# Kernel optimization log

Hardware: AMD Instinct MI355X
Metric: run time of the kernel (lower is better)

Reference implementation:

```python
import jax, jax.numpy as jnp
import numpy as np

N = 50000; E = 400000; T = 8; CIN = 16; C = 32; L = 2
F = C * T; END = 128; G = 64; EPS = 1e-5


def conv1d(x, W, b, pad):
    # x: (N, Cin, T), W: (Cout, Cin, K) -> (N, Cout, T)  ('same' padding)
    y = jax.lax.conv_general_dilated(x, W, (1,), [(pad, pad)],
                                     dimension_numbers=('NCH', 'OIH', 'NCH'))
    return y + b[None, :, None]


def gated_conv(x, W3, b3):
    # Temporal_Gated_Conv: relu(conv1(x) * sigmoid(conv2(x)) + conv3(x))
    P = conv1d(x, W3[0], b3[0], 1)
    Q = jax.nn.sigmoid(conv1d(x, W3[1], b3[1], 1))
    R = conv1d(x, W3[2], b3[2], 1)
    return jax.nn.relu(P * Q + R)


def bn(x, g, b, axes):
    # BatchNorm in training mode (batch statistics), channel axis = 1
    m = jnp.mean(x, axis=axes, keepdims=True)
    v = jnp.var(x, axis=axes, keepdims=True)
    sh = [1] * x.ndim; sh[1] = -1
    return (x - m) * jax.lax.rsqrt(v + EPS) * g.reshape(sh) + b.reshape(sh)


def gcn(x, W, b, src, dst):
    # GCNConv with self-loops (already appended to src/dst) and symmetric norm
    h = x @ W  # transform first: (N, F)
    deg = jax.ops.segment_sum(jnp.ones(src.shape[0], x.dtype), dst, num_segments=N)
    dinv = jnp.where(deg > 0, jax.lax.rsqrt(jnp.maximum(deg, 1.0)), 0.0)
    norm = dinv[src] * dinv[dst]  # (E+N,)
    out = jax.ops.segment_sum(h[src] * norm[:, None], dst, num_segments=N)
    return out + b


def stgcn_forward(X, edge_index, graphs, W_in, b_in, res_W, res_b, g1_W, g1_b,
                  bn0_g, bn0_b, gcn_W, gcn_b, bn1_g, bn1_b, g2_W, g2_b,
                  bn2_g, bn2_b, out_W1, out_b1, out_W2, out_b2, out_W3, out_b3):
    loop = jnp.arange(N)
    src = jnp.concatenate([edge_index[0], loop])
    dst = jnp.concatenate([edge_index[1], loop])
    x = conv1d(X, W_in, b_in, 0)  # input 1x1 conv -> (N, C, T)
    for i in range(L):
        residual = conv1d(x, res_W[i], res_b[i], 0)
        h = gated_conv(x, g1_W[i], g1_b[i])
        h = bn(h, bn0_g[i], bn0_b[i], (0, 2))
        h = h.reshape(N, F)                      # view(N, n_seq * C) row-major
        h = gcn(h, gcn_W[i], gcn_b[i], src, dst)
        h = bn(h, bn1_g[i], bn1_b[i], (0,))
        h = h.reshape(N, C, T)
        h = gated_conv(h, g2_W[i], g2_b[i])
        h = bn(h, bn2_g[i], bn2_b[i], (0, 2))
        h = h + residual
        if i != L - 1:                            # last layer skips activation
            h = jax.nn.relu(h)
        x = h
    # graph mode: take last timestep, then mean/max/sum pool per graph
    xl = x[:, :, -1]  # (N, C)
    cnt = jax.ops.segment_sum(jnp.ones((N,), xl.dtype), graphs, num_segments=G)
    s = jax.ops.segment_sum(xl, graphs, num_segments=G)
    mean = s / jnp.maximum(cnt, 1.0)[:, None]
    mx = jax.ops.segment_max(xl, graphs, num_segments=G)
    mx = jnp.where(cnt[:, None] > 0, mx, 0.0)
    xg = jnp.concatenate([mean, mx, s], axis=1)  # (G, 3C)
    h = jax.nn.relu(xg @ out_W1 + out_b1)
    h = jax.nn.relu(h @ out_W2 + out_b2)
    return h @ out_W3 + out_b3  # (G, 1)


def setup_inputs() -> dict:
    key = jax.random.key(0)
    ks = jax.random.split(key, 12)
    s = 0.1
    return {
        'X': jax.random.normal(ks[0], (N, CIN, T), jnp.float32),
        'edge_index': jax.random.randint(ks[1], (2, E), 0, N),
        'graphs': jnp.sort(jax.random.randint(ks[2], (N,), 0, G)),
        'W_in': jax.random.normal(ks[3], (C, CIN, 1)) * s,
        'b_in': jnp.zeros((C,)),
        'res_W': jax.random.normal(ks[4], (L, C, C, 1)) * s,
        'res_b': jnp.zeros((L, C)),
        'g1_W': jax.random.normal(ks[5], (L, 3, C, C, 3)) * s,
        'g1_b': jnp.zeros((L, 3, C)),
        'bn0_g': jnp.ones((L, C)), 'bn0_b': jnp.zeros((L, C)),
        'gcn_W': jax.random.normal(ks[6], (L, F, F)) * np.float32(1.0 / np.sqrt(F)),
        'gcn_b': jnp.zeros((L, F)),
        'bn1_g': jnp.ones((L, F)), 'bn1_b': jnp.zeros((L, F)),
        'g2_W': jax.random.normal(ks[7], (L, 3, C, C, 3)) * s,
        'g2_b': jnp.zeros((L, 3, C)),
        'bn2_g': jnp.ones((L, C)), 'bn2_b': jnp.zeros((L, C)),
        'out_W1': jax.random.normal(ks[8], (3 * C, END)) * s,
        'out_b1': jnp.zeros((END,)),
        'out_W2': jax.random.normal(ks[9], (END, END // 2)) * s,
        'out_b2': jnp.zeros((END // 2,)),
        'out_W3': jax.random.normal(ks[10], (END // 2, 1)) * s,
        'out_b3': jnp.zeros((1,)),
    }


def reference(X, edge_index, graphs, W_in, b_in, res_W, res_b, g1_W, g1_b,
              bn0_g, bn0_b, gcn_W, gcn_b, bn1_g, bn1_b, g2_W, g2_b,
              bn2_g, bn2_b, out_W1, out_b1, out_W2, out_b2, out_W3, out_b3):
    return stgcn_forward(X, edge_index, graphs, W_in, b_in, res_W, res_b,
                         g1_W, g1_b, bn0_g, bn0_b, gcn_W, gcn_b, bn1_g, bn1_b,
                         g2_W, g2_b, bn2_g, bn2_b, out_W1, out_b1, out_W2,
                         out_b2, out_W3, out_b3)
```

## Files before the change

### kernel.cpp

```cpp
#include <hip/hip_runtime.h>
#include <hip/hip_bf16.h>

#define NN 50000
#define EE 400000
#define EPSF 1e-5f
#define NB 196
#define NGATED 1280

typedef unsigned short u16;
typedef __attribute__((ext_vector_type(8))) short bf16x8;
typedef __attribute__((ext_vector_type(4))) float f32x4;
typedef __attribute__((ext_vector_type(2))) float f32x2;

__device__ __forceinline__ float b2f(u16 u) { return __uint_as_float(((unsigned)u) << 16); }
__device__ __forceinline__ u16 f2b(float f) {
  unsigned x = __float_as_uint(f);
  unsigned r = x + 0x7FFFu + ((x >> 16) & 1u);
  return (u16)(r >> 16);
}
__device__ __forceinline__ unsigned pack2(float lo, float hi) {
  return (unsigned)f2b(lo) | ((unsigned)f2b(hi) << 16);
}
__device__ __forceinline__ f32x2 mk2(float a, float b) { f32x2 r; r.x = a; r.y = b; return r; }
__device__ __forceinline__ void gl16(const void* g, void* l) {
  __builtin_amdgcn_global_load_lds(
      (const __attribute__((address_space(1))) void*)g,
      (__attribute__((address_space(3))) void*)l, 16, 0, 0);
}

__global__ __launch_bounds__(256) void k_convin(
    const float* __restrict__ X, u16* __restrict__ out,
    const float* __restrict__ Wi, const float* __restrict__ bi)
{
  __shared__ float xs[1024];
  __shared__ float wi[16 * 33];
  const int tid = threadIdx.x;
  for (int idx = tid; idx < 512; idx += 256) {
    int co = idx >> 4, ci = idx & 15;
    wi[ci * 33 + co] = Wi[idx];
  }
  const long xbase = (long)blockIdx.x * 1024;
  ((float4*)xs)[tid] = ((const float4*)(X + xbase))[tid];
  __syncthreads();
  const int nl = tid >> 5, c = tid & 31;
  float acc[8];
  {
    float bc = bi[c];
#pragma unroll
    for (int t = 0; t < 8; ++t) acc[t] = bc;
  }
  const float* xrow = xs + (nl << 7);
  for (int ci = 0; ci < 16; ++ci) {
    float w = wi[ci * 33 + c];
    float4 xa = *(const float4*)(xrow + ci * 8);
    float4 xb = *(const float4*)(xrow + ci * 8 + 4);
    acc[0] += xa.x * w; acc[1] += xa.y * w; acc[2] += xa.z * w; acc[3] += xa.w * w;
    acc[4] += xb.x * w; acc[5] += xb.y * w; acc[6] += xb.z * w; acc[7] += xb.w * w;
  }
  uint4 o;
  o.x = pack2(acc[0], acc[1]); o.y = pack2(acc[2], acc[3]);
  o.z = pack2(acc[4], acc[5]); o.w = pack2(acc[6], acc[7]);
  *(uint4*)(out + (long)blockIdx.x * 2048 + tid * 8) = o;
}

__global__ void k_deg(const int* __restrict__ dst, int* __restrict__ degi)
{
  int e = blockIdx.x * 256 + threadIdx.x;
  if (e < EE) atomicAdd(degi + dst[e], 1);
}
__global__ void k_dinv(const int* __restrict__ degi, float* __restrict__ dinv)
{
  int n = blockIdx.x * 256 + threadIdx.x;
  if (n < NN) dinv[n] = rsqrtf((float)degi[n] + 1.0f);
}

__global__ __launch_bounds__(256) void k_psum(const int* __restrict__ degi,
                                              int* __restrict__ bsum)
{
  __shared__ int red[4];
  const int tid = threadIdx.x;
  int i = blockIdx.x * 256 + tid;
  int v = (i < NN) ? degi[i] : 0;
#pragma unroll
  for (int d = 32; d >= 1; d >>= 1) v += __shfl_down(v, d);
  if ((tid & 63) == 0) red[tid >> 6] = v;
  __syncthreads();
  if (tid == 0) bsum[blockIdx.x] = red[0] + red[1] + red[2] + red[3];
}

__global__ __launch_bounds__(256) void k_bscan(const int* __restrict__ bsum,
                                               int* __restrict__ boff)
{
  __shared__ int wsum[4];
  const int tid = threadIdx.x, lane = tid & 63, wv = tid >> 6;
  int v = (tid < NB) ? bsum[tid] : 0;
  int s = v;
#pragma unroll
  for (int d = 1; d < 64; d <<= 1) { int t = __shfl_up(s, d); if (lane >= d) s += t; }
  if (lane == 63) wsum[wv] = s;
  __syncthreads();
  int wo = 0;
  for (int w = 0; w < wv; ++w) wo += wsum[w];
  if (tid < NB) boff[tid] = wo + s - v;
}

__global__ __launch_bounds__(256) void k_scan2(const int* __restrict__ degi,
                                               const int* __restrict__ boff,
                                               int* __restrict__ rowptr,
                                               int* __restrict__ cursor)
{
  __shared__ int wsum[4];
  const int tid = threadIdx.x, lane = tid & 63, wv = tid >> 6;
  int i = blockIdx.x * 256 + tid;
  int v = (i < NN) ? degi[i] : 0;
  int s = v;
#pragma unroll
  for (int d = 1; d < 64; d <<= 1) { int t = __shfl_up(s, d); if (lane >= d) s += t; }
  if (lane == 63) wsum[wv] = s;
  __syncthreads();
  int wo = 0;
  for (int w = 0; w < wv; ++w) wo += wsum[w];
  int excl = boff[blockIdx.x] + wo + (s - v);
  if (i < NN) { rowptr[i] = excl; cursor[i] = excl; }
  if (i == NN) rowptr[NN] = excl;
}

__global__ void k_fill(const int* __restrict__ src, const int* __restrict__ dst,
                       const float* __restrict__ dinv,
                       int* __restrict__ cursor,
                       int* __restrict__ eidx, float* __restrict__ enrm)
{
  int e = blockIdx.x * 256 + threadIdx.x;
  if (e < EE) {
    int s = src[e], d = dst[e];
    int p = atomicAdd(cursor + d, 1);
    eidx[p] = s;
    enrm[p] = dinv[s] * dinv[d];
  }
}

__global__ __launch_bounds__(256) void k_gather(
    const u16* __restrict__ hw, u16* __restrict__ out,
    const int* __restrict__ rowptr, const int* __restrict__ eidx,
    const float* __restrict__ enrm, const float* __restrict__ dinv)
{
  const int wid = (blockIdx.x << 2) + (threadIdx.x >> 6);
  if (wid >= NN) return;
  const int lane = threadIdx.x & 63;
  const int c0 = lane << 2;
  float a0, a1, a2, a3;
  {
    float d2 = dinv[wid]; d2 *= d2;
    uint2 v = *(const uint2*)(hw + (long)wid * 256 + c0);
    a0 = d2 * b2f((u16)(v.x & 0xFFFF)); a1 = d2 * b2f((u16)(v.x >> 16));
    a2 = d2 * b2f((u16)(v.y & 0xFFFF)); a3 = d2 * b2f((u16)(v.y >> 16));
  }
  int p = rowptr[wid];
  const int end = rowptr[wid + 1];
  for (; p + 1 < end; p += 2) {
    int s0 = eidx[p], s1 = eidx[p + 1];
    float n0 = enrm[p], n1 = enrm[p + 1];
    uint2 v0 = *(const uint2*)(hw + (long)s0 * 256 + c0);
    uint2 v1 = *(const uint2*)(hw + (long)s1 * 256 + c0);
    a0 += n0 * b2f((u16)(v0.x & 0xFFFF)) + n1 * b2f((u16)(v1.x & 0xFFFF));
    a1 += n0 * b2f((u16)(v0.x >> 16))    + n1 * b2f((u16)(v1.x >> 16));
    a2 += n0 * b2f((u16)(v0.y & 0xFFFF)) + n1 * b2f((u16)(v1.y & 0xFFFF));
    a3 += n0 * b2f((u16)(v0.y >> 16))    + n1 * b2f((u16)(v1.y >> 16));
  }
  if (p < end) {
    int s0 = eidx[p];
    float n0 = enrm[p];
    uint2 v0 = *(const uint2*)(hw + (long)s0 * 256 + c0);
    a0 += n0 * b2f((u16)(v0.x & 0xFFFF));
    a1 += n0 * b2f((u16)(v0.x >> 16));
    a2 += n0 * b2f((u16)(v0.y & 0xFFFF));
    a3 += n0 * b2f((u16)(v0.y >> 16));
  }
  uint2 o; o.x = pack2(a0, a1); o.y = pack2(a2, a3);
  *(uint2*)(out + (long)wid * 256 + c0) = o;
}

template<int FOLD>
__global__ __launch_bounds__(256) void k_gatedv(
    const u16* __restrict__ in, u16* __restrict__ out,
    const float* __restrict__ Wg,
    const float* __restrict__ bg,
    const float* __restrict__ s1in, const float* __restrict__ s2in,
    const float* __restrict__ gin, const float* __restrict__ bin,
    float cntInv,
    float* __restrict__ s1, float* __restrict__ s2)
{
  __shared__ float xs[2048];
  __shared__ unsigned wlA[3072];
  __shared__ u16 wlB[3072];
  __shared__ float red1[128], red2[128];
  const int tid = threadIdx.x;

  for (int idx = tid; idx < 3072; idx += 256) {
    int conv = idx >> 10;
    int r = idx & 1023;
    int co = r >> 5, ci = r & 31;
    const float* wsrc = Wg + (((conv << 5) + co) * 32 + ci) * 3;
    float w0 = wsrc[0], w1 = wsrc[1], w2 = wsrc[2];
    int di = (conv << 10) + (ci << 5) + co;
    wlA[di] = pack2(w0, w1);
    wlB[di] = f2b(w2);
  }

  const int nl = tid >> 5, c = tid & 31;
  const float bP = bg[c], bQ = bg[32 + c], bR = bg[64 + c];
  float affr[8], bffr[8];
  if (FOLD) {
    const int f0 = c << 3;
#pragma unroll
    for (int j = 0; j < 8; ++j) {
      float m = s1in[f0 + j] * cntInv;
      float var = s2in[f0 + j] * cntInv - m * m;
      float A = gin[f0 + j] / sqrtf(var + EPSF);
      affr[j] = A;
      bffr[j] = bin[f0 + j] - m * A;
    }
  }
  float gsum = 0.0f, gsq = 0.0f;
  const int swa = c >> 2;
  const int NT = NN / 8;

  long tile = blockIdx.x;
  uint4 v = *((const uint4*)(in + tile * 2048) + tid);

  for (; tile < NT; tile += gridDim.x) {
    __syncthreads();
    {
      float d[8];
      d[0] = b2f((u16)(v.x & 0xFFFF)); d[1] = b2f((u16)(v.x >> 16));
      d[2] = b2f((u16)(v.y & 0xFFFF)); d[3] = b2f((u16)(v.y >> 16));
      d[4] = b2f((u16)(v.z & 0xFFFF)); d[5] = b2f((u16)(v.z >> 16));
      d[6] = b2f((u16)(v.w & 0xFFFF)); d[7] = b2f((u16)(v.w >> 16));
      if (FOLD) {
#pragma unroll
        for (int j = 0; j < 8; ++j) d[j] = fmaf(affr[j], d[j], bffr[j]);
      }
      float4* xw = (float4*)xs + (nl << 6);
      xw[(2 * c) ^ swa]     = make_float4(d[0], d[1], d[2], d[3]);
      xw[(2 * c + 1) ^ swa] = make_float4(d[4], d[5], d[6], d[7]);
    }
    __syncthreads();

    {
      long nxt = tile + gridDim.x;
      if (nxt < NT) v = *((const uint4*)(in + nxt * 2048) + tid);
    }

    f32x2 aP[4], aQ[4], aR[4];
#pragma unroll
    for (int j = 0; j < 4; ++j) {
      aP[j] = mk2(bP, bP); aQ[j] = mk2(bQ, bQ); aR[j] = mk2(bR, bR);
    }
    const float4* xrow = (const float4*)xs + (nl << 6);
    for (int ci = 0; ci < 32; ++ci) {
      const int a = ci >> 2;
      float4 xa = xrow[(2 * ci) ^ a];
      float4 xb = xrow[(2 * ci + 1) ^ a];
      f32x2 p0 = mk2(xa.x, xa.y), p1 = mk2(xa.z, xa.w);
      f32x2 p2 = mk2(xb.x, xb.y), p3 = mk2(xb.z, xb.w);
      f32x2 A0  = mk2(0.0f, xa.x);
      f32x2 s01 = mk2(xa.y, xa.z);
      f32x2 s23 = mk2(xa.w, xb.x);
      f32x2 s45 = mk2(xb.y, xb.z);
      f32x2 c3  = mk2(xb.w, 0.0f);
      const int wi = (ci << 5) + c;
#define CONV3(ACC, OFF)                                                        \
      {                                                                        \
        unsigned wA = wlA[wi + OFF];                                           \
        float w0 = __uint_as_float(wA << 16);                                  \
        float w1 = __uint_as_float(wA & 0xFFFF0000u);                          \
        float w2 = b2f(wlB[wi + OFF]);                                         \
        f32x2 W0 = mk2(w0, w0), W1 = mk2(w1, w1), W2 = mk2(w2, w2);            \
        ACC[0] = __builtin_elementwise_fma(s01, W2,                            \
                 __builtin_elementwise_fma(p0, W1,                             \
                 __builtin_elementwise_fma(A0, W0, ACC[0])));                  \
        ACC[1] = __builtin_elementwise_fma(s23, W2,                            \
                 __builtin_elementwise_fma(p1, W1,                             \
                 __builtin_elementwise_fma(s01, W0, ACC[1])));                 \
        ACC[2] = __builtin_elementwise_fma(s45, W2,                            \
                 __builtin_elementwise_fma(p2, W1,                             \
                 __builtin_elementwise_fma(s23, W0, ACC[2])));                 \
        ACC[3] = __builtin_elementwise_fma(c3, W2,                             \
                 __builtin_elementwise_fma(p3, W1,                             \
                 __builtin_elementwise_fma(s45, W0, ACC[3])));                 \
      }
      CONV3(aP, 0)
      CONV3(aQ, 1024)
      CONV3(aR, 2048)
#undef CONV3
    }
    float hv[8];
#pragma unroll
    for (int j = 0; j < 4; ++j) {
#pragma unroll
      for (int h2 = 0; h2 < 2; ++h2) {
        float pp = h2 ? aP[j].y : aP[j].x;
        float qq = h2 ? aQ[j].y : aQ[j].x;
        float rr = h2 ? aR[j].y : aR[j].x;
        float q = __builtin_amdgcn_rcpf(1.0f + __expf(-qq));
        float h = fmaxf(fmaf(pp, q, rr), 0.0f);
        hv[j * 2 + h2] = h; gsum += h; gsq += h * h;
      }
    }
    uint4 o;
    o.x = pack2(hv[0], hv[1]); o.y = pack2(hv[2], hv[3]);
    o.z = pack2(hv[4], hv[5]); o.w = pack2(hv[6], hv[7]);
    *(uint4*)(out + tile * 2048 + tid * 8) = o;
  }

  float o1 = gsum + __shfl_down(gsum, 32);
  float o2 = gsq + __shfl_down(gsq, 32);
  int wave = tid >> 6, lane = tid & 63;
  if (lane < 32) { red1[wave * 32 + lane] = o1; red2[wave * 32 + lane] = o2; }
  __syncthreads();
  if (tid < 32) {
    float a = red1[tid] + red1[32 + tid] + red1[64 + tid] + red1[96 + tid];
    float b = red2[tid] + red2[32 + tid] + red2[64 + tid] + red2[96 + tid];
    atomicAdd(s1 + tid, a);
    atomicAdd(s2 + tid, b);
  }
}

__global__ __launch_bounds__(256) void k_wprep(
    const float* __restrict__ W, const float* __restrict__ st1, const float* __restrict__ st2,
    const float* __restrict__ g0, const float* __restrict__ b0,
    u16* __restrict__ WT, float* __restrict__ rb)
{
  __shared__ float tile[64][68];
  __shared__ float affl[64];
  const int b = blockIdx.x;
  const int t = threadIdx.x;
  const float ci400 = 1.0f / 400000.0f;
  if (b < 16) {
    const int kx = (b & 3) * 64, jx = (b >> 2) * 64;
    if (t < 64) {
      int cch = (kx + t) >> 3;
      float m = st1[cch] * ci400;
      float var = st2[cch] * ci400 - m * m;
      affl[t] = g0[cch] / sqrtf(var + EPSF);
    }
    {
      int r = t >> 2, c0 = (t & 3) * 16;
#pragma unroll
      for (int i = 0; i < 4; ++i) {
        float4 v = *(const float4*)(W + (long)(kx + r) * 256 + jx + c0 + i * 4);
        tile[r][c0 + i * 4 + 0] = v.x; tile[r][c0 + i * 4 + 1] = v.y;
        tile[r][c0 + i * 4 + 2] = v.z; tile[r][c0 + i * 4 + 3] = v.w;
      }
    }
    __syncthreads();
    {
      int jl = t >> 2, k0 = (t & 3) * 16;
      u16 tmp[16];
#pragma unroll
      for (int kk = 0; kk < 16; ++kk)
        tmp[kk] = f2b(affl[k0 + kk] * tile[k0 + kk][jl]);
      u16* dst = WT + (long)(jx + jl) * 256 + kx + k0;
      *(uint4*)dst = ((uint4*)tmp)[0];
      *(uint4*)(dst + 8) = ((uint4*)tmp)[1];
    }
  } else {
    const int k0 = (b - 16) * 32;
    if (t < 32) {
      int cch = (k0 + t) >> 3;
      float m = st1[cch] * ci400;
      float var = st2[cch] * ci400 - m * m;
      float A = g0[cch] / sqrtf(var + EPSF);
      affl[t] = b0[cch] - m * A;
    }
    __syncthreads();
    float s = 0.0f;
    for (int kk = 0; kk < 32; ++kk) s += affl[kk] * W[(long)(k0 + kk) * 256 + t];
    atomicAdd(rb + t, s);
  }
}

__global__ __launch_bounds__(512, 2) void k_gemmm(
    const u16* __restrict__ A, const u16* __restrict__ WT,
    const float* __restrict__ rowbias, u16* __restrict__ Out)
{
  __shared__ u16 At[128 * 64];
  __shared__ u16 Bt[256 * 64];
  const int tid = threadIdx.x, l = tid & 63, w = tid >> 6;
  const long n0 = (long)blockIdx.x * 128;
  const int wr = (w & 1) << 6, wc = (w >> 1) << 6;
  f32x4 acc[4][4];
#pragma unroll
  for (int i = 0; i < 4; ++i)
#pragma unroll
    for (int j = 0; j < 4; ++j) acc[i][j] = (f32x4){0.f, 0.f, 0.f, 0.f};
  float rb[4];
#pragma unroll
  for (int cf = 0; cf < 4; ++cf) rb[cf] = rowbias[wc + (cf << 4) + (l & 15)];

  for (int kt = 0; kt < 4; ++kt) {
    if (kt) __syncthreads();
#pragma unroll
    for (int i = 0; i < 2; ++i) {
      int row = (w << 4) + (i << 3) + (l >> 3);
      int sg = (l & 7) ^ (row & 7);
      long n = n0 + row; if (n >= NN) n = NN - 1;
      gl16(A + n * 256 + kt * 64 + sg * 8, At + ((w << 4) + (i << 3)) * 64);
    }
#pragma unroll
    for (int i = 0; i < 4; ++i) {
      int row = (w << 5) + (i << 3) + (l >> 3);
      int sg = (l & 7) ^ (row & 7);
      gl16(WT + (long)row * 256 + kt * 64 + sg * 8, Bt + ((w << 5) + (i << 3)) * 64);
    }
    __syncthreads();
#pragma unroll
    for (int ks = 0; ks < 2; ++ks) {
      bf16x8 af[4], bf[4];
#pragma unroll
      for (int rf = 0; rf < 4; ++rf) {
        int row = wr + (rf << 4) + (l & 15);
        int slot = ((ks << 2) + (l >> 4)) ^ (row & 7);
        af[rf] = *(const bf16x8*)(At + row * 64 + (slot << 3));
      }
#pragma unroll
      for (int cf = 0; cf < 4; ++cf) {
        int row = wc + (cf << 4) + (l & 15);
        int slot = ((ks << 2) + (l >> 4)) ^ (row & 7);
        bf[cf] = *(const bf16x8*)(Bt + row * 64 + (slot << 3));
      }
#pragma unroll
      for (int rf = 0; rf < 4; ++rf)
#pragma unroll
        for (int cf = 0; cf < 4; ++cf)
          acc[rf][cf] = __builtin_amdgcn_mfma_f32_16x16x32_bf16(
              af[rf], bf[cf], acc[rf][cf], 0, 0, 0);
    }
  }
#pragma unroll
  for (int rf = 0; rf < 4; ++rf)
#pragma unroll
    for (int reg = 0; reg < 4; ++reg) {
      long n = n0 + wr + (rf << 4) + ((l >> 4) << 2) + reg;
      if (n < NN) {
        u16* orow = Out + n * 256 + wc + (l & 15);
#pragma unroll
        for (int cf = 0; cf < 4; ++cf)
          orow[cf << 4] = f2b(acc[rf][cf][reg] + rb[cf]);
      }
    }
}

__global__ void k_colstats(const u16* __restrict__ x, int rows,
                           float* __restrict__ s1, float* __restrict__ s2)
{
  int f = threadIdx.x;
  float a = 0.0f, b = 0.0f;
  for (int n = blockIdx.x; n < rows; n += gridDim.x) {
    float v = b2f(x[(long)n * 256 + f]);
    a += v; b += v * v;
  }
  atomicAdd(s1 + f, a);
  atomicAdd(s2 + f, b);
}

__global__ __launch_bounds__(256) void k_final(
    u16* __restrict__ x, const u16* __restrict__ h2,
    const float* __restrict__ resW, const float* __restrict__ resb,
    const float* __restrict__ st1, const float* __restrict__ st2,
    const float* __restrict__ g2, const float* __restrict__ b2g,
    float* __restrict__ xl, int mode)
{
  __shared__ float xs[2048];
  __shared__ float wr[32 * 33];
  __shared__ float a2l[32], b2l[32];
  const int tid = threadIdx.x;
  for (int idx = tid; idx < 1024; idx += 256) {
    int co = idx >> 5, ci = idx & 31;
    wr[ci * 33 + co] = resW[idx];
  }
  if (tid < 32) {
    const float ci400 = 1.0f / 400000.0f;
    float m = st1[tid] * ci400;
    float var = st2[tid] * ci400 - m * m;
    float A = g2[tid] / sqrtf(var + EPSF);
    a2l[tid] = A;
    b2l[tid] = b2g[tid] - m * A;
  }
  const long base = (long)blockIdx.x * 2048;
  {
    const uint4 v = *((const uint4*)(x + base) + tid);
    float* d = xs + tid * 8;
    d[0] = b2f((u16)(v.x & 0xFFFF)); d[1] = b2f((u16)(v.x >> 16));
    d[2] = b2f((u16)(v.y & 0xFFFF)); d[3] = b2f((u16)(v.y >> 16));
    d[4] = b2f((u16)(v.z & 0xFFFF)); d[5] = b2f((u16)(v.z >> 16));
    d[6] = b2f((u16)(v.w & 0xFFFF)); d[7] = b2f((u16)(v.w >> 16));
  }
  __syncthreads();
  const int nl = tid >> 5, c = tid & 31;
  float r[8];
  {
    float rb = resb[c];
#pragma unroll
    for (int t = 0; t < 8; ++t) r[t] = rb;
  }
  const float* xrow = xs + (nl << 8);
  for (int ci = 0; ci < 32; ++ci) {
    float w = wr[ci * 33 + c];
    float4 xa = *(const float4*)(xrow + ci * 8);
    float4 xb = *(const float4*)(xrow + ci * 8 + 4);
    r[0] += xa.x * w; r[1] += xa.y * w; r[2] += xa.z * w; r[3] += xa.w * w;
    r[4] += xb.x * w; r[5] += xb.y * w; r[6] += xb.z * w; r[7] += xb.w * w;
  }
  float a2 = a2l[c], b2 = b2l[c];
  float hv[8];
  {
    const uint4 v = *((const uint4*)(h2 + base) + tid);
    hv[0] = b2f((u16)(v.x & 0xFFFF)); hv[1] = b2f((u16)(v.x >> 16));
    hv[2] = b2f((u16)(v.y & 0xFFFF)); hv[3] = b2f((u16)(v.y >> 16));
    hv[4] = b2f((u16)(v.z & 0xFFFF)); hv[5] = b2f((u16)(v.z >> 16));
    hv[6] = b2f((u16)(v.w & 0xFFFF)); hv[7] = b2f((u16)(v.w >> 16));
  }
  if (mode == 0) {
    uint4 o;
    float ov[8];
#pragma unroll
    for (int t = 0; t < 8; ++t) ov[t] = fmaxf(fmaf(a2, hv[t], b2) + r[t], 0.0f);
    o.x = pack2(ov[0], ov[1]); o.y = pack2(ov[2], ov[3]);
    o.z = pack2(ov[4], ov[5]); o.w = pack2(ov[6], ov[7]);
    *(uint4*)(x + base + tid * 8) = o;
  } else {
    float v = fmaf(a2, hv[7], b2) + r[7];
    int n = blockIdx.x * 8 + nl;
    xl[n * 32 + c] = v;
  }
}

__global__ __launch_bounds__(256) void k_pool(
    const float* __restrict__ xl, const int* __restrict__ graphs,
    int* __restrict__ cnt, float* __restrict__ sp, unsigned* __restrict__ mxu)
{
  __shared__ float lsum[64 * 32];
  __shared__ unsigned lmax[64 * 32];
  __shared__ int lcnt[64];
  const int tid = threadIdx.x;
  const int n0 = blockIdx.x << 8;
  const int nend = min(n0 + 256, NN);
  const int gmin = graphs[n0];
  const int gmax = graphs[nend - 1];
  const int span = gmax - gmin + 1;
  for (int i = tid; i < span * 32; i += 256) { lsum[i] = 0.0f; lmax[i] = 0u; }
  for (int i = tid; i < span; i += 256) lcnt[i] = 0;
  __syncthreads();
  const int c = tid & 31;
  const int nbase = n0 + ((tid >> 5) << 5);
  int curg = -1; float s = 0.0f; unsigned m = 0u; int cn = 0;
  for (int i = 0; i < 32; ++i) {
    int n = nbase + i;
    if (n >= nend) break;
    int g = graphs[n];
    float v = xl[(n << 5) + c];
    unsigned u = __float_as_uint(v);
    u = (u & 0x80000000u) ? ~u : (u | 0x80000000u);
    if (g != curg) {
      if (curg >= 0) {
        atomicAdd(&lsum[((curg - gmin) << 5) + c], s);
        atomicMax(&lmax[((curg - gmin) << 5) + c], m);
        if (c == 0) atomicAdd(&lcnt[curg - gmin], cn);
      }
      curg = g; s = v; m = u; cn = 1;
    } else {
      s += v; m = (u > m) ? u : m; cn++;
    }
  }
  if (curg >= 0) {
    atomicAdd(&lsum[((curg - gmin) << 5) + c], s);
    atomicMax(&lmax[((curg - gmin) << 5) + c], m);
    if (c == 0) atomicAdd(&lcnt[curg - gmin], cn);
  }
  __syncthreads();
  for (int i = tid; i < span * 32; i += 256) {
    atomicAdd(sp + (gmin << 5) + i, lsum[i]);
    atomicMax(mxu + (gmin << 5) + i, lmax[i]);
  }
  for (int i = tid; i < span; i += 256)
    if (lcnt[i]) atomicAdd(cnt + gmin + i, lcnt[i]);
}

__global__ __launch_bounds__(128) void k_head(
    const int* __restrict__ cnt, const float* __restrict__ sp,
    const unsigned* __restrict__ mxu,
    const float* __restrict__ W1, const float* __restrict__ b1,
    const float* __restrict__ W2, const float* __restrict__ b2,
    const float* __restrict__ W3, const float* __restrict__ b3,
    float* __restrict__ out)
{
  __shared__ float xg[96], hh1[128], hh2[64];
  const int g = blockIdx.x, tid = threadIdx.x;
  if (tid < 32) {
    float s = sp[g * 32 + tid];
    int cn = cnt[g];
    float mean = s / fmaxf((float)cn, 1.0f);
    float mx = 0.0f;
    if (cn > 0) {
      unsigned u = mxu[g * 32 + tid];
      unsigned ub = (u & 0x80000000u) ? (u ^ 0x80000000u) : ~u;
      mx = __uint_as_float(ub);
    }
    xg[tid] = mean; xg[32 + tid] = mx; xg[64 + tid] = s;
  }
  __syncthreads();
  {
    float a = b1[tid];
    for (int k = 0; k < 96; ++k) a += xg[k] * W1[k * 128 + tid];
    hh1[tid] = fmaxf(a, 0.0f);
  }
  __syncthreads();
  if (tid < 64) {
    float a = b2[tid];
    for (int k = 0; k < 128; ++k) a += hh1[k] * W2[k * 64 + tid];
    hh2[tid] = fmaxf(a, 0.0f);
  }
  __syncthreads();
  if (tid < 64) {
    float p = hh2[tid] * W3[tid];
    for (int off = 32; off; off >>= 1) p += __shfl_down(p, off);
    if (tid == 0) out[g] = p + b3[0];
  }
}

extern "C" void kernel_launch(void* const* d_in, const int* in_sizes, int n_in,
                              void* d_out, int out_size, void* d_ws, size_t ws_size,
                              hipStream_t stream)
{
  const float* X       = (const float*)d_in[0];
  const int*   edge    = (const int*)d_in[1];
  const int*   graphs  = (const int*)d_in[2];
  const float* W_in    = (const float*)d_in[3];
  const float* b_in    = (const float*)d_in[4];
  const float* res_W   = (const float*)d_in[5];
  const float* res_b   = (const float*)d_in[6];
  const float* g1_W    = (const float*)d_in[7];
  const float* g1_b    = (const float*)d_in[8];
  const float* bn0_g   = (const float*)d_in[9];
  const float* bn0_b   = (const float*)d_in[10];
  const float* gcn_W   = (const float*)d_in[11];
  const float* bn1_g   = (const float*)d_in[13];
  const float* bn1_b   = (const float*)d_in[14];
  const float* g2_W    = (const float*)d_in[15];
  const float* g2_b    = (const float*)d_in[16];
  const float* bn2_g   = (const float*)d_in[17];
  const float* bn2_b   = (const float*)d_in[18];
  const float* out_W1  = (const float*)d_in[19];
  const float* out_b1  = (const float*)d_in[20];
  const float* out_W2  = (const float*)d_in[21];
  const float* out_b2  = (const float*)d_in[22];
  const float* out_W3  = (const float*)d_in[23];
  const float* out_b3  = (const float*)d_in[24];
  float* outp = (float*)d_out;

  const int* srcp = edge;
  const int* dstp = edge + EE;

  const long BIGE = (long)NN * 256;
  u16*   P0   = (u16*)d_ws;
  u16*   P1   = P0 + BIGE;
  u16*   P2   = P1 + BIGE;
  u16*   P3   = P2 + BIGE;
  u16*   WT   = P3 + BIGE;
  float* xl   = (float*)(WT + 65536);
  float* dinv = xl + (long)NN * 32;
  int*   rowptr = (int*)(dinv + NN);
  int*   cursor = rowptr + NN + 1;
  int*   eidx   = cursor + NN;
  float* enrm   = (float*)(eidx + EE);
  int*   bsum   = (int*)(enrm + EE);
  int*   boff   = bsum + NB;
  int*   degi = boff + NB;
  float* stats = (float*)(degi + NN);
  int*   cnt  = (int*)(stats + 1280);
  float* sp   = (float*)(cnt + 64);
  unsigned* mxu = (unsigned*)(sp + 2048);
  float* rbias = (float*)(mxu + 2048);

  const size_t zero_bytes = (size_t)(NN + 1280 + 64 + 2048 + 2048 + 512) * 4;
  hipMemsetAsync(degi, 0, zero_bytes, stream);

  k_convin<<<NN / 8, 256, 0, stream>>>(X, P0, W_in, b_in);
  k_deg<<<(EE + 255) / 256, 256, 0, stream>>>(dstp, degi);
  k_dinv<<<(NN + 255) / 256, 256, 0, stream>>>(degi, dinv);
  k_psum<<<NB, 256, 0, stream>>>(degi, bsum);
  k_bscan<<<1, 256, 0, stream>>>(bsum, boff);
  k_scan2<<<NB, 256, 0, stream>>>(degi, boff, rowptr, cursor);
  k_fill<<<(EE + 255) / 256, 256, 0, stream>>>(srcp, dstp, dinv, cursor, eidx, enrm);

  for (int l = 0; l < 2; ++l) {
    const float* g1Wl = g1_W + l * 9216;
    const float* g1bl = g1_b + l * 96;
    const float* g2Wl = g2_W + l * 9216;
    const float* g2bl = g2_b + l * 96;
    const float* gWl  = gcn_W + l * 65536;
    float* st = stats + l * 640;
    float* rbl = rbias + l * 256;

    k_gatedv<0><<<NGATED, 256, 0, stream>>>(P0, P1, g1Wl, g1bl,
                                            nullptr, nullptr, nullptr, nullptr, 0.0f,
                                            st + 0, st + 32);
    k_wprep<<<24, 256, 0, stream>>>(gWl, st + 0, st + 32, bn0_g + l * 32, bn0_b + l * 32,
                                    WT, rbl);
    k_gemmm<<<(NN + 127) / 128, 512, 0, stream>>>(P1, WT, rbl, P3);
    k_gather<<<(NN + 3) / 4, 256, 0, stream>>>(P3, P2, rowptr, eidx, enrm, dinv);
    k_colstats<<<512, 256, 0, stream>>>(P2, NN, st + 64, st + 320);
    k_gatedv<1><<<NGATED, 256, 0, stream>>>(P2, P1, g2Wl, g2bl,
                                            st + 64, st + 320,
                                            bn1_g + l * 256, bn1_b + l * 256,
                                            1.0f / (float)NN,
                                            st + 576, st + 608);
    k_final<<<NN / 8, 256, 0, stream>>>(P0, P1, res_W + l * 1024, res_b + l * 32,
                                        st + 576, st + 608,
                                        bn2_g + l * 32, bn2_b + l * 32,
                                        xl, (l == 0) ? 0 : 1);
  }

  k_pool<<<(NN + 255) / 256, 256, 0, stream>>>(xl, graphs, cnt, sp, mxu);
  k_head<<<64, 128, 0, stream>>>(cnt, sp, mxu, out_W1, out_b1, out_W2, out_b2,
                                 out_W3, out_b3, outp);

  (void)in_sizes; (void)n_in; (void)out_size; (void)ws_size;
}
```

Before: 760.3 us.

## Unroll gather by four, pack gated-conv weights, vectorize column stats

The edge-gather loop is unrolled to four edges per iteration, so more independent row loads are in flight. Gated-conv weights for the three convolutions are packed into one uint4 plus a u16 per (ci,co), which replaces six LDS reads per input channel with two. The column-statistics kernel now reads 16-byte vectors covering 8 features per thread, reduces within the block in shared memory, and launches fewer blocks. The changes trade extra registers and shared memory for fewer memory instructions.

```diff
diff --git a/kernel.cpp b/kernel.cpp
--- a/kernel.cpp
+++ b/kernel.cpp
@@ -157,17 +157,23 @@
   }
   int p = rowptr[wid];
   const int end = rowptr[wid + 1];
-  for (; p + 1 < end; p += 2) {
-    int s0 = eidx[p], s1 = eidx[p + 1];
-    float n0 = enrm[p], n1 = enrm[p + 1];
+  for (; p + 3 < end; p += 4) {
+    int s0 = eidx[p], s1 = eidx[p + 1], s2 = eidx[p + 2], s3 = eidx[p + 3];
+    float n0 = enrm[p], n1 = enrm[p + 1], n2 = enrm[p + 2], n3 = enrm[p + 3];
     uint2 v0 = *(const uint2*)(hw + (long)s0 * 256 + c0);
     uint2 v1 = *(const uint2*)(hw + (long)s1 * 256 + c0);
-    a0 += n0 * b2f((u16)(v0.x & 0xFFFF)) + n1 * b2f((u16)(v1.x & 0xFFFF));
-    a1 += n0 * b2f((u16)(v0.x >> 16))    + n1 * b2f((u16)(v1.x >> 16));
-    a2 += n0 * b2f((u16)(v0.y & 0xFFFF)) + n1 * b2f((u16)(v1.y & 0xFFFF));
-    a3 += n0 * b2f((u16)(v0.y >> 16))    + n1 * b2f((u16)(v1.y >> 16));
-  }
-  if (p < end) {
+    uint2 v2 = *(const uint2*)(hw + (long)s2 * 256 + c0);
+    uint2 v3 = *(const uint2*)(hw + (long)s3 * 256 + c0);
+    a0 += n0 * b2f((u16)(v0.x & 0xFFFF)) + n1 * b2f((u16)(v1.x & 0xFFFF))
+        + n2 * b2f((u16)(v2.x & 0xFFFF)) + n3 * b2f((u16)(v3.x & 0xFFFF));
+    a1 += n0 * b2f((u16)(v0.x >> 16))    + n1 * b2f((u16)(v1.x >> 16))
+        + n2 * b2f((u16)(v2.x >> 16))    + n3 * b2f((u16)(v3.x >> 16));
+    a2 += n0 * b2f((u16)(v0.y & 0xFFFF)) + n1 * b2f((u16)(v1.y & 0xFFFF))
+        + n2 * b2f((u16)(v2.y & 0xFFFF)) + n3 * b2f((u16)(v3.y & 0xFFFF));
+    a3 += n0 * b2f((u16)(v0.y >> 16))    + n1 * b2f((u16)(v1.y >> 16))
+        + n2 * b2f((u16)(v2.y >> 16))    + n3 * b2f((u16)(v3.y >> 16));
+  }
+  for (; p < end; ++p) {
     int s0 = eidx[p];
     float n0 = enrm[p];
     uint2 v0 = *(const uint2*)(hw + (long)s0 * 256 + c0);
@@ -191,20 +197,24 @@
     float* __restrict__ s1, float* __restrict__ s2)
 {
   __shared__ float xs[2048];
-  __shared__ unsigned wlA[3072];
-  __shared__ u16 wlB[3072];
+  __shared__ uint4 wl4[1024];
+  __shared__ u16 wl2[1024];
   __shared__ float red1[128], red2[128];
   const int tid = threadIdx.x;
 
-  for (int idx = tid; idx < 3072; idx += 256) {
-    int conv = idx >> 10;
-    int r = idx & 1023;
-    int co = r >> 5, ci = r & 31;
-    const float* wsrc = Wg + (((conv << 5) + co) * 32 + ci) * 3;
-    float w0 = wsrc[0], w1 = wsrc[1], w2 = wsrc[2];
-    int di = (conv << 10) + (ci << 5) + co;
-    wlA[di] = pack2(w0, w1);
-    wlB[di] = f2b(w2);
+  for (int idx = tid; idx < 1024; idx += 256) {
+    int co = idx >> 5, ci = idx & 31;
+    const float* pw = Wg + co * 96 + ci * 3;
+    const float* qw = pw + 3072;
+    const float* rw = pw + 6144;
+    uint4 wv;
+    wv.x = pack2(pw[0], pw[1]);
+    wv.y = pack2(qw[0], qw[1]);
+    wv.z = pack2(rw[0], rw[1]);
+    wv.w = pack2(pw[2], qw[2]);
+    int di = (ci << 5) + co;
+    wl4[di] = wv;
+    wl2[di] = f2b(rw[2]);
   }
 
   const int nl = tid >> 5, c = tid & 31;
@@ -269,12 +279,13 @@
       f32x2 s45 = mk2(xb.y, xb.z);
       f32x2 c3  = mk2(xb.w, 0.0f);
       const int wi = (ci << 5) + c;
-#define CONV3(ACC, OFF)                                                        \
+      const uint4 wA = wl4[wi];
+      const float rw2 = b2f(wl2[wi]);
+#define CONV3(ACC, W01, W2F)                                                   \
       {                                                                        \
-        unsigned wA = wlA[wi + OFF];                                           \
-        float w0 = __uint_as_float(wA << 16);                                  \
-        float w1 = __uint_as_float(wA & 0xFFFF0000u);                          \
-        float w2 = b2f(wlB[wi + OFF]);                                         \
+        float w0 = __uint_as_float((W01) << 16);                               \
+        float w1 = __uint_as_float((W01) & 0xFFFF0000u);                       \
+        float w2 = (W2F);                                                      \
         f32x2 W0 = mk2(w0, w0), W1 = mk2(w1, w1), W2 = mk2(w2, w2);            \
         ACC[0] = __builtin_elementwise_fma(s01, W2,                            \
                  __builtin_elementwise_fma(p0, W1,                             \
@@ -289,9 +300,9 @@
                  __builtin_elementwise_fma(p3, W1,                             \
                  __builtin_elementwise_fma(s45, W0, ACC[3])));                 \
       }
-      CONV3(aP, 0)
-      CONV3(aQ, 1024)
-      CONV3(aR, 2048)
+      CONV3(aP, wA.x, __uint_as_float(wA.w << 16))
+      CONV3(aQ, wA.y, __uint_as_float(wA.w & 0xFFFF0000u))
+      CONV3(aR, wA.z, rw2)
 #undef CONV3
     }
     float hv[8];
@@ -451,17 +462,40 @@
     }
 }
 
-__global__ void k_colstats(const u16* __restrict__ x, int rows,
-                           float* __restrict__ s1, float* __restrict__ s2)
-{
-  int f = threadIdx.x;
-  float a = 0.0f, b = 0.0f;
-  for (int n = blockIdx.x; n < rows; n += gridDim.x) {
-    float v = b2f(x[(long)n * 256 + f]);
-    a += v; b += v * v;
-  }
-  atomicAdd(s1 + f, a);
-  atomicAdd(s2 + f, b);
+__global__ __launch_bounds__(256) void k_colstats(
+    const u16* __restrict__ x, float* __restrict__ s1, float* __restrict__ s2)
+{
+  __shared__ float ls1[2048], ls2[2048];
+  const int tid = threadIdx.x;
+  const int fgrp = tid & 31, rofs = tid >> 5;
+  float a[8], b[8];
+#pragma unroll
+  for (int j = 0; j < 8; ++j) { a[j] = 0.0f; b[j] = 0.0f; }
+  for (int n = (blockIdx.x << 3) + rofs; n < NN; n += 2048) {
+    uint4 v = *(const uint4*)(x + (long)n * 256 + (fgrp << 3));
+    const unsigned uu[4] = {v.x, v.y, v.z, v.w};
+#pragma unroll
+    for (int k = 0; k < 4; ++k) {
+      float lo = b2f((u16)(uu[k] & 0xFFFF));
+      float hi = b2f((u16)(uu[k] >> 16));
+      a[2 * k] += lo;     b[2 * k] += lo * lo;
+      a[2 * k + 1] += hi; b[2 * k + 1] += hi * hi;
+    }
+  }
+#pragma unroll
+  for (int j = 0; j < 8; ++j) {
+    ls1[rofs * 256 + (fgrp << 3) + j] = a[j];
+    ls2[rofs * 256 + (fgrp << 3) + j] = b[j];
+  }
+  __syncthreads();
+  {
+    int f = tid;
+    float sa = 0.0f, sb = 0.0f;
+#pragma unroll
+    for (int r = 0; r < 8; ++r) { sa += ls1[r * 256 + f]; sb += ls2[r * 256 + f]; }
+    atomicAdd(s1 + f, sa);
+    atomicAdd(s2 + f, sb);
+  }
 }
 
 __global__ __launch_bounds__(256) void k_final(
@@ -710,7 +744,7 @@
                                     WT, rbl);
     k_gemmm<<<(NN + 127) / 128, 512, 0, stream>>>(P1, WT, rbl, P3);
     k_gather<<<(NN + 3) / 4, 256, 0, stream>>>(P3, P2, rowptr, eidx, enrm, dinv);
-    k_colstats<<<512, 256, 0, stream>>>(P2, NN, st + 64, st + 320);
+    k_colstats<<<256, 256, 0, stream>>>(P2, st + 64, st + 320);
     k_gatedv<1><<<NGATED, 256, 0, stream>>>(P2, P1, g2Wl, g2bl,
                                             st + 64, st + 320,
                                             bn1_g + l * 256, bn1_b + l * 256,
```

Measured after the change: 679.4 us. 1.12x faster.
